# Performance work log

Hardware: AMD Instinct MI355X
Metric: run time of the kernel (lower is better)

## Reference

```python
import jax, jax.numpy as jnp
import numpy as np

B, S, D = 2, 2048, 1024
H = 16
DK = D // H
DFF = 4096
EPS = 1e-6


def rotate_half(x):
    x1, x2 = jnp.split(x, 2, axis=-1)
    return jnp.concatenate((-x2, x1), axis=-1)


def build_rope(dim, seq_len):
    inv_freq = 1.0 / (10000.0 ** (jnp.arange(0, dim, 2, dtype=jnp.float32) / dim))
    t = jnp.arange(seq_len, dtype=jnp.float32)
    freqs = jnp.einsum('i,j->ij', t, inv_freq)
    emb = jnp.concatenate((freqs, freqs), axis=-1)
    return jnp.cos(emb)[None, None], jnp.sin(emb)[None, None]  # [1,1,S,dk]


def rmsnorm(x, g):
    rms = jnp.sqrt(jnp.mean(x * x, axis=-1, keepdims=True) + EPS)
    return x / rms * g


def setup_inputs() -> dict:
    key = jax.random.key(0)
    ks = jax.random.split(key, 10)
    sc = 0.02
    x = jax.random.normal(ks[0], (B, S, D), dtype=jnp.float32)
    mask = jnp.tril(jnp.ones((S, S), dtype=jnp.int32))[None, None]  # causal [1,1,S,S]
    wq = jax.random.normal(ks[1], (D, D), dtype=jnp.float32) * sc
    wk = jax.random.normal(ks[2], (D, D), dtype=jnp.float32) * sc
    wv = jax.random.normal(ks[3], (D, D), dtype=jnp.float32) * sc
    wo = jax.random.normal(ks[4], (D, D), dtype=jnp.float32) * sc
    w1 = jax.random.normal(ks[5], (2 * DFF, D), dtype=jnp.float32) * sc
    w2 = jax.random.normal(ks[6], (D, DFF), dtype=jnp.float32) * sc
    g1 = jnp.ones((D,), dtype=jnp.float32)
    g2 = jnp.ones((D,), dtype=jnp.float32)
    return {"x": x, "mask": mask, "wq": wq, "wk": wk, "wv": wv, "wo": wo,
            "w1": w1, "w2": w2, "g1": g1, "g2": g2}


def decoder_block(x, mask, wq, wk, wv, wo, w1, w2, g1, g2):
    b, s, d = x.shape
    # --- self-attention sublayer ---
    h = rmsnorm(x, g1)
    q = (h @ wq.T).reshape(b, s, H, DK).transpose(0, 2, 1, 3)
    k = (h @ wk.T).reshape(b, s, H, DK).transpose(0, 2, 1, 3)
    v = (h @ wv.T).reshape(b, s, H, DK).transpose(0, 2, 1, 3)
    cos, sin = build_rope(DK, s)
    q = q * cos + rotate_half(q) * sin
    k = k * cos + rotate_half(k) * sin
    scores = jnp.einsum('bhqd,bhkd->bhqk', q, k) / jnp.sqrt(jnp.float32(DK))
    scores = jnp.where(mask == 0, jnp.float32(-1e9), scores)
    p = jax.nn.softmax(scores, axis=-1)
    ctx = jnp.einsum('bhqk,bhkd->bhqd', p, v)
    ctx = ctx.transpose(0, 2, 1, 3).reshape(b, s, d)
    x = x + ctx @ wo.T
    # --- SwiGLU FFN sublayer ---
    h2 = rmsnorm(x, g2)
    u = h2 @ w1.T  # [b,s,2*DFF]
    u1, u2 = jnp.split(u, 2, axis=-1)
    ffn = (u1 * jax.nn.silu(u2)) @ w2.T
    return x + ffn


def reference(x, mask, wq, wk, wv, wo, w1, w2, g1, g2):
    return decoder_block(x, mask, wq, wk, wv, wo, w1, w2, g1, g2)
```

## Files before the change

kernel.cpp:

```cpp
#include <hip/hip_runtime.h>
#include <hip/hip_bf16.h>

#define BB 2
#define SS 2048
#define DD 1024
#define NH 16
#define DKH 64
#define DFF 4096
#define MTOK (BB*SS)

typedef __hip_bfloat16 bf16;
typedef __attribute__((ext_vector_type(8))) short s16x8;
typedef __attribute__((ext_vector_type(4))) float f32x4;

__device__ __forceinline__ float bs2f(short s) {
    unsigned int u = ((unsigned int)(unsigned short)s) << 16;
    return __uint_as_float(u);
}
__device__ __forceinline__ float b2f(bf16 v) { return __bfloat162float(v); }
__device__ __forceinline__ bf16 f2b(float v) { return __float2bfloat16(v); }
__device__ __forceinline__ short f2bs(float v) {
    bf16 b = __float2bfloat16(v);
    return *(short*)&b;
}

__device__ __forceinline__ void load16(const bf16* g, bf16* l) {
    __builtin_amdgcn_global_load_lds((const __attribute__((address_space(1))) void*)g,
                                     (__attribute__((address_space(3))) void*)l,
                                     16, 0, 0);
}


__global__ void cvt_kernel(const float* __restrict__ src, bf16* __restrict__ dst) {
    const int i = blockIdx.x * blockDim.x + threadIdx.x;
    float4 v = ((const float4*)src)[i];
    short4 o;
    o.x = f2bs(v.x); o.y = f2bs(v.y); o.z = f2bs(v.z); o.w = f2bs(v.w);
    ((short4*)dst)[i] = o;
}

__global__ void cvt4_kernel(const float* __restrict__ s0, const float* __restrict__ s1,
                            const float* __restrict__ s2, const float* __restrict__ s3,
                            bf16* __restrict__ dst) {
    const int z = blockIdx.z;
    const float* src = (z == 0) ? s0 : (z == 1) ? s1 : (z == 2) ? s2 : s3;
    const int i = blockIdx.x * blockDim.x + threadIdx.x;
    float4 v = ((const float4*)src)[i];
    short4 o;
    o.x = f2bs(v.x); o.y = f2bs(v.y); o.z = f2bs(v.z); o.w = f2bs(v.w);
    ((short4*)(dst + (size_t)z * DD * DD))[i] = o;
}

__global__ void rmsnorm_kernel(const float* __restrict__ x, const float* __restrict__ g,
                               bf16* __restrict__ out) {
    const int row = blockIdx.x;
    const int tid = threadIdx.x;
    float4 xv = ((const float4*)(x + (size_t)row * DD))[tid];
    float ss = xv.x*xv.x + xv.y*xv.y + xv.z*xv.z + xv.w*xv.w;
    #pragma unroll
    for (int off = 32; off > 0; off >>= 1) ss += __shfl_down(ss, off);
    __shared__ float red[4];
    const int wv = tid >> 6, lane = tid & 63;
    if (lane == 0) red[wv] = ss;
    __syncthreads();
    const float tot = red[0] + red[1] + red[2] + red[3];
    const float inv = rsqrtf(tot * (1.0f / DD) + 1e-6f);
    float4 gv = ((const float4*)g)[tid];
    short4 o;
    o.x = f2bs(xv.x * inv * gv.x);
    o.y = f2bs(xv.y * inv * gv.y);
    o.z = f2bs(xv.z * inv * gv.z);
    o.w = f2bs(xv.w * inv * gv.w);
    ((short4*)(out + (size_t)row * DD))[tid] = o;
}

__global__ __launch_bounds__(256) void gemm_qkv(const bf16* __restrict__ A,
                                                const bf16* __restrict__ Wbase,
                                                bf16* __restrict__ Obase) {
    __shared__ bf16 As[128 * 32];
    __shared__ bf16 Bs[128 * 32];
    const int tid = threadIdx.x, lane = tid & 63, wv = tid >> 6;
    const int col = lane & 15, quad = lane >> 4;
    const int wm = wv >> 1, wn = wv & 1;
    const int m0 = blockIdx.y * 128;
    const int n0 = blockIdx.x * 128;
    const bf16* W = Wbase + (size_t)blockIdx.z * DD * DD;
    bf16* C = Obase + (size_t)blockIdx.z * MTOK * DD;

    const int srow = tid >> 2;
    const int scol = (((tid & 3) ^ (srow & 3))) * 8;
    const bf16* Ag = A + (size_t)(m0 + srow) * DD + scol;
    const bf16* Wg = W + (size_t)(n0 + srow) * DD + scol;
    bf16* Asl = As + tid * 8;
    bf16* Bsl = Bs + tid * 8;
    const size_t half = (size_t)64 * DD;
    const int rg = (quad ^ (col & 3)) * 8;

    f32x4 acc[4][4] = {};
    for (int k0 = 0; k0 < DD; k0 += 32) {
        __syncthreads();
        load16(Ag + k0,        Asl);
        load16(Ag + half + k0, Asl + 2048);
        load16(Wg + k0,        Bsl);
        load16(Wg + half + k0, Bsl + 2048);
        __syncthreads();
        s16x8 af[4], bfr[4];
        #pragma unroll
        for (int t = 0; t < 4; t++) {
            af[t]  = *(const s16x8*)(As + (wm * 64 + t * 16 + col) * 32 + rg);
            bfr[t] = *(const s16x8*)(Bs + (wn * 64 + t * 16 + col) * 32 + rg);
        }
        #pragma unroll
        for (int tm = 0; tm < 4; tm++)
            #pragma unroll
            for (int tn = 0; tn < 4; tn++)
                acc[tm][tn] = __builtin_amdgcn_mfma_f32_16x16x32_bf16(af[tm], bfr[tn], acc[tm][tn], 0, 0, 0);
    }
    #pragma unroll
    for (int tm = 0; tm < 4; tm++)
        #pragma unroll
        for (int tn = 0; tn < 4; tn++)
            #pragma unroll
            for (int r = 0; r < 4; r++) {
                const int rr = m0 + wm * 64 + tm * 16 + quad * 4 + r;
                const int cc = n0 + wn * 64 + tn * 16 + col;
                C[(size_t)rr * DD + cc] = f2b(acc[tm][tn][r]);
            }
}

__global__ __launch_bounds__(256) void gemm128_atomic(const bf16* __restrict__ A,
                                                      const bf16* __restrict__ W,
                                                      float* C, int N, int K, int KC) {
    __shared__ bf16 As[128 * 32];
    __shared__ bf16 Bs[128 * 32];
    const int tid = threadIdx.x, lane = tid & 63, wv = tid >> 6;
    const int col = lane & 15, quad = lane >> 4;
    const int wm = wv >> 1, wn = wv & 1;
    const int m0 = blockIdx.y * 128;
    const int n0 = blockIdx.x * 128;
    const int koff = blockIdx.z * KC;

    const int srow = tid >> 2;
    const int scol = (((tid & 3) ^ (srow & 3))) * 8;
    const bf16* Ag = A + (size_t)(m0 + srow) * K + scol;
    const bf16* Wg = W + (size_t)(n0 + srow) * K + scol;
    bf16* Asl = As + tid * 8;
    bf16* Bsl = Bs + tid * 8;
    const size_t half = (size_t)64 * K;
    const int rg = (quad ^ (col & 3)) * 8;

    f32x4 acc[4][4] = {};
    for (int k0 = koff; k0 < koff + KC; k0 += 32) {
        __syncthreads();
        load16(Ag + k0,        Asl);
        load16(Ag + half + k0, Asl + 2048);
        load16(Wg + k0,        Bsl);
        load16(Wg + half + k0, Bsl + 2048);
        __syncthreads();
        s16x8 af[4], bfr[4];
        #pragma unroll
        for (int t = 0; t < 4; t++) {
            af[t]  = *(const s16x8*)(As + (wm * 64 + t * 16 + col) * 32 + rg);
            bfr[t] = *(const s16x8*)(Bs + (wn * 64 + t * 16 + col) * 32 + rg);
        }
        #pragma unroll
        for (int tm = 0; tm < 4; tm++)
            #pragma unroll
            for (int tn = 0; tn < 4; tn++)
                acc[tm][tn] = __builtin_amdgcn_mfma_f32_16x16x32_bf16(af[tm], bfr[tn], acc[tm][tn], 0, 0, 0);
    }
    #pragma unroll
    for (int tm = 0; tm < 4; tm++)
        #pragma unroll
        for (int tn = 0; tn < 4; tn++)
            #pragma unroll
            for (int r = 0; r < 4; r++) {
                const int rr = m0 + wm * 64 + tm * 16 + quad * 4 + r;
                const int cc = n0 + wn * 64 + tn * 16 + col;
                atomicAdd(&C[(size_t)rr * N + cc], acc[tm][tn][r]);
            }
}

__global__ __launch_bounds__(256) void gemm64n_f32res(const bf16* __restrict__ A,
                                                      const bf16* __restrict__ W,
                                                      const float* res, float* C,
                                                      int M, int N, int K) {
    __shared__ bf16 As[128 * 32];
    __shared__ bf16 Bs[64 * 32];
    const int tid = threadIdx.x, lane = tid & 63, wv = tid >> 6;
    const int col = lane & 15, quad = lane >> 4;
    const int wm = wv >> 1, wn = wv & 1;
    const int m0 = blockIdx.y * 128;
    const int n0 = blockIdx.x * 64;

    const int srow = tid >> 2;
    const int scol = (((tid & 3) ^ (srow & 3))) * 8;
    const bf16* Ag = A + (size_t)(m0 + srow) * K + scol;
    const bf16* Wg = W + (size_t)(n0 + srow) * K + scol;
    bf16* Asl = As + tid * 8;
    bf16* Bsl = Bs + tid * 8;
    const size_t half = (size_t)64 * K;
    const int rg = (quad ^ (col & 3)) * 8;

    f32x4 acc[4][2] = {};
    for (int k0 = 0; k0 < K; k0 += 32) {
        __syncthreads();
        load16(Ag + k0,        Asl);
        load16(Ag + half + k0, Asl + 2048);
        load16(Wg + k0,        Bsl);
        __syncthreads();
        s16x8 af[4], bfr[2];
        #pragma unroll
        for (int t = 0; t < 4; t++)
            af[t] = *(const s16x8*)(As + (wm * 64 + t * 16 + col) * 32 + rg);
        #pragma unroll
        for (int t = 0; t < 2; t++)
            bfr[t] = *(const s16x8*)(Bs + (wn * 32 + t * 16 + col) * 32 + rg);
        #pragma unroll
        for (int tm = 0; tm < 4; tm++)
            #pragma unroll
            for (int tn = 0; tn < 2; tn++)
                acc[tm][tn] = __builtin_amdgcn_mfma_f32_16x16x32_bf16(af[tm], bfr[tn], acc[tm][tn], 0, 0, 0);
    }
    #pragma unroll
    for (int tm = 0; tm < 4; tm++)
        #pragma unroll
        for (int tn = 0; tn < 2; tn++)
            #pragma unroll
            for (int r = 0; r < 4; r++) {
                const int rr = m0 + wm * 64 + tm * 16 + quad * 4 + r;
                const int cc = n0 + wn * 32 + tn * 16 + col;
                C[(size_t)rr * N + cc] = acc[tm][tn][r] + res[(size_t)rr * N + cc];
            }
}

__device__ __forceinline__ void stage_sw(const bf16* Ag, const bf16* Wg0, const bf16* Wg1,
                                         bf16* Asl, bf16* Bsl, int k0) {
    load16(Ag + k0,                        Asl);
    load16(Ag + k0 + 32,                   Asl + 8192);
    load16(Ag + (size_t)128 * DD + k0,     Asl + 4096);
    load16(Ag + (size_t)128 * DD + k0 + 32, Asl + 8192 + 4096);
    load16(Wg0 + k0,                       Bsl);
    load16(Wg0 + k0 + 32,                  Bsl + 8192);
    load16(Wg1 + k0,                       Bsl + 4096);
    load16(Wg1 + k0 + 32,                  Bsl + 8192 + 4096);
}

__device__ __forceinline__ void compute_sw(const bf16* Ab, const bf16* Bb,
                                           f32x4 (*acc)[4],
                                           int wm, int wn, int col, int quad) {
    const int rg = (quad ^ (col & 3)) * 8;
    #pragma unroll
    for (int kk = 0; kk < 2; kk++) {
        const bf16* Ap = Ab + kk * 8192;
        const bf16* Bp = Bb + kk * 8192;
        s16x8 af[8], bfr[4];
        #pragma unroll
        for (int t = 0; t < 8; t++)
            af[t] = *(const s16x8*)(Ap + (wm * 128 + t * 16 + col) * 32 + rg);
        #pragma unroll
        for (int t = 0; t < 4; t++)
            bfr[t] = *(const s16x8*)(Bp + (wn * 64 + t * 16 + col) * 32 + rg);
        #pragma unroll
        for (int tm = 0; tm < 8; tm++)
            #pragma unroll
            for (int tn = 0; tn < 4; tn++)
                acc[tm][tn] = __builtin_amdgcn_mfma_f32_16x16x32_bf16(af[tm], bfr[tn], acc[tm][tn], 0, 0, 0);
    }
}

__global__ __launch_bounds__(512, 2) void gemm256_swiglu(const bf16* __restrict__ A,
                                                         const bf16* __restrict__ W,
                                                         bf16* __restrict__ G) {
    __shared__ bf16 As[2][2][256 * 32];
    __shared__ bf16 Bs[2][2][256 * 32];
    const int tid = threadIdx.x, lane = tid & 63, wv = tid >> 6;
    const int col = lane & 15, quad = lane >> 4;
    const int wm = wv >> 2, wn = wv & 3;
    const int m0 = blockIdx.y * 256;
    const int n0 = blockIdx.x * 128;

    const int srow = tid >> 2;
    const int scol = ((tid & 3) ^ (srow & 3)) * 8;
    const bf16* Ag = A + (size_t)(m0 + srow) * DD + scol;
    const int r0 = srow, r1 = srow + 128;
    const int wr0 = n0 + ((r0 >> 6) << 5) + (r0 & 31) + (((r0 >> 5) & 1) ? DFF : 0);
    const int wr1 = n0 + ((r1 >> 6) << 5) + (r1 & 31) + (((r1 >> 5) & 1) ? DFF : 0);
    const bf16* Wg0 = W + (size_t)wr0 * DD + scol;
    const bf16* Wg1 = W + (size_t)wr1 * DD + scol;
    bf16* Asl = &As[0][0][0] + tid * 8;
    bf16* Bsl = &Bs[0][0][0] + tid * 8;
    const int bufoff = 2 * 8192;

    f32x4 acc[8][4] = {};

    stage_sw(Ag, Wg0, Wg1, Asl, Bsl, 0);
    __syncthreads();
    int buf = 0;
    for (int t = 0; t < 15; t++) {
        stage_sw(Ag, Wg0, Wg1, Asl + (buf ^ 1) * bufoff, Bsl + (buf ^ 1) * bufoff,
                 (t + 1) * 64);
        compute_sw(&As[buf][0][0], &Bs[buf][0][0], acc, wm, wn, col, quad);
        __syncthreads();
        buf ^= 1;
    }
    compute_sw(&As[buf][0][0], &Bs[buf][0][0], acc, wm, wn, col, quad);

    #pragma unroll
    for (int tm = 0; tm < 8; tm++)
        #pragma unroll
        for (int tn = 0; tn < 2; tn++)
            #pragma unroll
            for (int r = 0; r < 4; r++) {
                const int rr = m0 + wm * 128 + tm * 16 + quad * 4 + r;
                const int cc = n0 + wn * 32 + tn * 16 + col;
                const float u1 = acc[tm][tn][r];
                const float u2 = acc[tm][tn + 2][r];
                const float sig = 1.0f / (1.0f + __expf(-u2));
                G[(size_t)rr * DFF + cc] = f2b(u1 * u2 * sig);
            }
}

__global__ void rope_kernel(bf16* __restrict__ q, bf16* __restrict__ k) {
    const int idx = blockIdx.x * blockDim.x + threadIdx.x;
    const int d = idx & 31;
    const int h = (idx >> 5) & (NH - 1);
    const int row = idx >> 9;
    const int s = row & (SS - 1);
    const float invf = powf(10000.0f, -(float)d * (1.0f / 32.0f));
    const float ang = (float)s * invf;
    float sn, cs;
    sincosf(ang, &sn, &cs);
    const size_t base = (size_t)row * DD + h * DKH + d;
    {
        float x1 = b2f(q[base]), x2 = b2f(q[base + 32]);
        q[base]      = f2b(x1 * cs - x2 * sn);
        q[base + 32] = f2b(x2 * cs + x1 * sn);
    }
    {
        float x1 = b2f(k[base]), x2 = b2f(k[base + 32]);
        k[base]      = f2b(x1 * cs - x2 * sn);
        k[base + 32] = f2b(x2 * cs + x1 * sn);
    }
}

__global__ __launch_bounds__(256) void vt_transpose(const bf16* __restrict__ v,
                                                    bf16* __restrict__ vt) {
    __shared__ short tile[64][72];
    const int s0 = blockIdx.x * 64;
    const int bh = blockIdx.y;
    const int b = bh >> 4, h = bh & 15;
    const bf16* src = v + (size_t)b * SS * DD + h * DKH;
    #pragma unroll
    for (int it = 0; it < 2; it++) {
        const int sl = (threadIdx.x >> 3) + it * 32;
        const int dp = (threadIdx.x & 7) * 8;
        s16x8 val = *(const s16x8*)(src + (size_t)(s0 + sl) * DD + dp);
        *(s16x8*)&tile[sl][dp] = val;
    }
    __syncthreads();
    bf16* dst = vt + (size_t)bh * DKH * SS;
    #pragma unroll
    for (int it = 0; it < 2; it++) {
        const int dk = (threadIdx.x >> 3) + it * 32;
        const int sp = (threadIdx.x & 7) * 8;
        s16x8 o;
        #pragma unroll
        for (int j = 0; j < 8; j++) o[j] = tile[sp + j][dk];
        *(s16x8*)(dst + (size_t)dk * SS + s0 + sp) = o;
    }
}

__device__ __forceinline__ void stage_kv(const bf16* kbase, const bf16* vtbase,
                                         bf16* Kd, bf16* Vd, int kt0, int tid) {
    const int row0 = tid >> 3;
    const int gl = tid & 7;
    #pragma unroll
    for (int r = 0; r < 2; r++) {
        const int row = row0 + r * 32;
        const int g = (gl ^ (row & 7)) * 8;
        load16(kbase + (size_t)(kt0 + row) * DD + g, Kd + tid * 8 + r * 2048);
        load16(vtbase + (size_t)row * SS + kt0 + g,  Vd + tid * 8 + r * 2048);
    }
}

__device__ __forceinline__ void attn_step(const bf16* Ks, const bf16* Vs,
                                          short (*pl)[72],
                                          s16x8 qf0, s16x8 qf1,
                                          f32x4* cacc, float* lacc,
                                          int col, int quad, int kt0, int q0w,
                                          bool need_mask) {
    f32x4 s4[4] = {};
    #pragma unroll
    for (int t = 0; t < 4; t++) {
        const int key = 16 * t + col;
        const int g0 = (quad ^ (key & 7)) * 8;
        s16x8 b0 = *(const s16x8*)(Ks + key * 64 + g0);
        s16x8 b1 = *(const s16x8*)(Ks + key * 64 + (g0 ^ 32));
        s4[t] = __builtin_amdgcn_mfma_f32_16x16x32_bf16(qf0, b0, s4[t], 0, 0, 0);
        s4[t] = __builtin_amdgcn_mfma_f32_16x16x32_bf16(qf1, b1, s4[t], 0, 0, 0);
    }
    #pragma unroll
    for (int t = 0; t < 4; t++)
        #pragma unroll
        for (int r = 0; r < 4; r++) {
            float sv = s4[t][r] * 0.125f;
            if (need_mask) {
                const int key = kt0 + 16 * t + col;
                const int qq  = q0w + quad * 4 + r;
                if (key > qq) sv = -1.0e30f;
            }
            const float p = __expf(sv);
            s4[t][r] = p;
            lacc[r] += p;
        }
    #pragma unroll
    for (int t = 0; t < 4; t++)
        #pragma unroll
        for (int r = 0; r < 4; r++)
            pl[quad * 4 + r][col + 16 * t] = f2bs(s4[t][r]);
    s16x8 pf0 = *(const s16x8*)&pl[col][quad * 8];
    s16x8 pf1 = *(const s16x8*)&pl[col][32 + quad * 8];
    #pragma unroll
    for (int tn = 0; tn < 4; tn++) {
        const int dk = 16 * tn + col;
        const int g0 = (quad ^ (dk & 7)) * 8;
        s16x8 b0 = *(const s16x8*)(Vs + dk * 64 + g0);
        s16x8 b1 = *(const s16x8*)(Vs + dk * 64 + (g0 ^ 32));
        cacc[tn] = __builtin_amdgcn_mfma_f32_16x16x32_bf16(pf0, b0, cacc[tn], 0, 0, 0);
        cacc[tn] = __builtin_amdgcn_mfma_f32_16x16x32_bf16(pf1, b1, cacc[tn], 0, 0, 0);
    }
}

__global__ __launch_bounds__(256) void attn_mfma2(const bf16* __restrict__ q,
                                                  const bf16* __restrict__ k,
                                                  const bf16* __restrict__ vt,
                                                  bf16* __restrict__ ctx) {
    __shared__ bf16 Ks[2][64 * 64];
    __shared__ bf16 Vs[2][64 * 64];
    __shared__ short plds[4][16][72];
    const int tid = threadIdx.x, lane = tid & 63, wv = tid >> 6;
    const int col = lane & 15, quad = lane >> 4;
    const int bh = blockIdx.y;
    const int b = bh >> 4, h = bh & 15;
    const int tA = blockIdx.x;
    const int tB = 31 - tA;
    const int q0A = tA * 64 + wv * 16;
    const int q0B = tB * 64 + wv * 16;

    const bf16* kbase  = k  + (size_t)b * SS * DD + h * DKH;
    const bf16* vtbase = vt + (size_t)bh * DKH * SS;

    const bf16* qrA = q + (size_t)(b * SS + q0A + col) * DD + h * DKH + quad * 8;
    const bf16* qrB = q + (size_t)(b * SS + q0B + col) * DD + h * DKH + quad * 8;
    s16x8 qfA0 = *(const s16x8*)(qrA);
    s16x8 qfA1 = *(const s16x8*)(qrA + 32);
    s16x8 qfB0 = *(const s16x8*)(qrB);
    s16x8 qfB1 = *(const s16x8*)(qrB + 32);

    f32x4 caccA[4] = {}, caccB[4] = {};
    float lA[4] = {}, lB[4] = {};

    const int last = tB;
    stage_kv(kbase, vtbase, Ks[0], Vs[0], 0, tid);
    int buf = 0;
    for (int kt = 0; kt <= last; kt++) {
        __syncthreads();
        if (kt < last)
            stage_kv(kbase, vtbase, Ks[buf ^ 1], Vs[buf ^ 1], (kt + 1) * 64, tid);
        const bf16* Kc = Ks[buf];
        const bf16* Vc = Vs[buf];
        if (kt <= tA)
            attn_step(Kc, Vc, plds[wv], qfA0, qfA1, caccA, lA,
                      col, quad, kt * 64, q0A, kt == tA);
        attn_step(Kc, Vc, plds[wv], qfB0, qfB1, caccB, lB,
                  col, quad, kt * 64, q0B, kt == tB);
        buf ^= 1;
    }
    #pragma unroll
    for (int r = 0; r < 4; r++) {
        #pragma unroll
        for (int off = 1; off < 16; off <<= 1) {
            lA[r] += __shfl_xor(lA[r], off);
            lB[r] += __shfl_xor(lB[r], off);
        }
    }
    #pragma unroll
    for (int tn = 0; tn < 4; tn++)
        #pragma unroll
        for (int r = 0; r < 4; r++) {
            const size_t tokA = (size_t)(b * SS + q0A + quad * 4 + r);
            ctx[tokA * DD + h * DKH + 16 * tn + col] = f2b(caccA[tn][r] / lA[r]);
            const size_t tokB = (size_t)(b * SS + q0B + quad * 4 + r);
            ctx[tokB * DD + h * DKH + 16 * tn + col] = f2b(caccB[tn][r] / lB[r]);
        }
}

extern "C" void kernel_launch(void* const* d_in, const int* in_sizes, int n_in,
                              void* d_out, int out_size, void* d_ws, size_t ws_size,
                              hipStream_t stream) {
    const float* x  = (const float*)d_in[0];
    const float* wq = (const float*)d_in[2];
    const float* wk = (const float*)d_in[3];
    const float* wv = (const float*)d_in[4];
    const float* wo = (const float*)d_in[5];
    const float* w1 = (const float*)d_in[6];
    const float* w2 = (const float*)d_in[7];
    const float* g1 = (const float*)d_in[8];
    const float* g2 = (const float*)d_in[9];
    float* out = (float*)d_out;
    char* ws = (char*)d_ws;

    const size_t MB = 1024 * 1024;
    bf16* hb   = (bf16*)(ws + 0 * MB);
    bf16* qb   = (bf16*)(ws + 8 * MB);
    bf16* kb   = (bf16*)(ws + 16 * MB);
    bf16* vb   = (bf16*)(ws + 24 * MB);
    bf16* ctxb = hb;
    bf16* h2b  = hb;
    bf16* gb   = qb;
    bf16* wqb  = (bf16*)(ws + 32 * MB);
    bf16* wob  = wqb + (size_t)3 * DD * DD;
    bf16* vtb  = (bf16*)(ws + 40 * MB);
    bf16* w1b  = (bf16*)(ws + 40 * MB);
    bf16* w2b  = (bf16*)(ws + 56 * MB);

    cvt4_kernel<<<dim3((DD * DD / 4) / 256, 1, 4), 256, 0, stream>>>(
        wq, wk, wv, wo, wqb);

    rmsnorm_kernel<<<MTOK, 256, 0, stream>>>(x, g1, hb);
    gemm_qkv<<<dim3(DD / 128, MTOK / 128, 3), 256, 0, stream>>>(hb, wqb, qb);

    vt_transpose<<<dim3(SS / 64, BB * NH), 256, 0, stream>>>(vb, vtb);
    rope_kernel<<<(BB * SS * NH * 32) / 256, 256, 0, stream>>>(qb, kb);

    attn_mfma2<<<dim3(16, BB * NH), 256, 0, stream>>>(qb, kb, vtb, ctxb);

    gemm64n_f32res<<<dim3(DD / 64, MTOK / 128), 256, 0, stream>>>(
        ctxb, wob, x, out, MTOK, DD, DD);
    rmsnorm_kernel<<<MTOK, 256, 0, stream>>>(out, g2, h2b);

    cvt_kernel<<<(2 * DFF * DD / 4) / 256, 256, 0, stream>>>(w1, w1b);
    cvt_kernel<<<(DD * DFF / 4) / 256, 256, 0, stream>>>(w2, w2b);

    gemm256_swiglu<<<dim3(DFF / 128, MTOK / 256), 512, 0, stream>>>(h2b, w1b, gb);
    gemm128_atomic<<<dim3(DD / 128, MTOK / 128, 2), 256, 0, stream>>>(
        gb, w2b, out, DD, DFF, DFF / 2);
}
```

Baseline: 440.5 us.

## Use 4-stage K32 LDS ring with vmcnt waits in SwiGLU GEMM

```diff
diff --git a/kernel.cpp b/kernel.cpp
--- a/kernel.cpp
+++ b/kernel.cpp
@@ -29,6 +29,8 @@
                                      (__attribute__((address_space(3))) void*)l,
                                      16, 0, 0);
 }
+
+#define WAITV(N) asm volatile("s_waitcnt vmcnt(" #N ")" ::: "memory")
 
 
 __global__ void cvt_kernel(const float* __restrict__ src, bf16* __restrict__ dst) {
@@ -234,46 +236,40 @@
             }
 }
 
-__device__ __forceinline__ void stage_sw(const bf16* Ag, const bf16* Wg0, const bf16* Wg1,
-                                         bf16* Asl, bf16* Bsl, int k0) {
-    load16(Ag + k0,                        Asl);
-    load16(Ag + k0 + 32,                   Asl + 8192);
-    load16(Ag + (size_t)128 * DD + k0,     Asl + 4096);
-    load16(Ag + (size_t)128 * DD + k0 + 32, Asl + 8192 + 4096);
-    load16(Wg0 + k0,                       Bsl);
-    load16(Wg0 + k0 + 32,                  Bsl + 8192);
-    load16(Wg1 + k0,                       Bsl + 4096);
-    load16(Wg1 + k0 + 32,                  Bsl + 8192 + 4096);
-}
-
-__device__ __forceinline__ void compute_sw(const bf16* Ab, const bf16* Bb,
-                                           f32x4 (*acc)[4],
-                                           int wm, int wn, int col, int quad) {
+__device__ __forceinline__ void stage_k32(const bf16* Ag, const bf16* Wg0,
+                                          const bf16* Wg1, bf16* Abuf, bf16* Bbuf,
+                                          int k0, int tid) {
+    load16(Ag + k0,                    Abuf + tid * 8);
+    load16(Ag + (size_t)128 * DD + k0, Abuf + tid * 8 + 4096);
+    load16(Wg0 + k0,                   Bbuf + tid * 8);
+    load16(Wg1 + k0,                   Bbuf + tid * 8 + 4096);
+}
+
+__device__ __forceinline__ void comp_k32(const bf16* Ap, const bf16* Bp,
+                                         f32x4 (*acc)[4],
+                                         int wm, int wn, int col, int quad) {
     const int rg = (quad ^ (col & 3)) * 8;
-    #pragma unroll
-    for (int kk = 0; kk < 2; kk++) {
-        const bf16* Ap = Ab + kk * 8192;
-        const bf16* Bp = Bb + kk * 8192;
-        s16x8 af[8], bfr[4];
-        #pragma unroll
-        for (int t = 0; t < 8; t++)
-            af[t] = *(const s16x8*)(Ap + (wm * 128 + t * 16 + col) * 32 + rg);
-        #pragma unroll
-        for (int t = 0; t < 4; t++)
-            bfr[t] = *(const s16x8*)(Bp + (wn * 64 + t * 16 + col) * 32 + rg);
-        #pragma unroll
-        for (int tm = 0; tm < 8; tm++)
-            #pragma unroll
-            for (int tn = 0; tn < 4; tn++)
-                acc[tm][tn] = __builtin_amdgcn_mfma_f32_16x16x32_bf16(af[tm], bfr[tn], acc[tm][tn], 0, 0, 0);
-    }
+    s16x8 af[8], bfr[4];
+    #pragma unroll
+    for (int t = 0; t < 8; t++)
+        af[t] = *(const s16x8*)(Ap + (wm * 128 + t * 16 + col) * 32 + rg);
+    #pragma unroll
+    for (int t = 0; t < 4; t++)
+        bfr[t] = *(const s16x8*)(Bp + (wn * 64 + t * 16 + col) * 32 + rg);
+    __builtin_amdgcn_s_setprio(1);
+    #pragma unroll
+    for (int tm = 0; tm < 8; tm++)
+        #pragma unroll
+        for (int tn = 0; tn < 4; tn++)
+            acc[tm][tn] = __builtin_amdgcn_mfma_f32_16x16x32_bf16(af[tm], bfr[tn], acc[tm][tn], 0, 0, 0);
+    __builtin_amdgcn_s_setprio(0);
 }
 
 __global__ __launch_bounds__(512, 2) void gemm256_swiglu(const bf16* __restrict__ A,
                                                          const bf16* __restrict__ W,
                                                          bf16* __restrict__ G) {
-    __shared__ bf16 As[2][2][256 * 32];
-    __shared__ bf16 Bs[2][2][256 * 32];
+    __shared__ bf16 As[4][256 * 32];
+    __shared__ bf16 Bs[4][256 * 32];
     const int tid = threadIdx.x, lane = tid & 63, wv = tid >> 6;
     const int col = lane & 15, quad = lane >> 4;
     const int wm = wv >> 2, wn = wv & 3;
@@ -288,23 +284,32 @@
     const int wr1 = n0 + ((r1 >> 6) << 5) + (r1 & 31) + (((r1 >> 5) & 1) ? DFF : 0);
     const bf16* Wg0 = W + (size_t)wr0 * DD + scol;
     const bf16* Wg1 = W + (size_t)wr1 * DD + scol;
-    bf16* Asl = &As[0][0][0] + tid * 8;
-    bf16* Bsl = &Bs[0][0][0] + tid * 8;
-    const int bufoff = 2 * 8192;
 
     f32x4 acc[8][4] = {};
 
-    stage_sw(Ag, Wg0, Wg1, Asl, Bsl, 0);
-    __syncthreads();
-    int buf = 0;
-    for (int t = 0; t < 15; t++) {
-        stage_sw(Ag, Wg0, Wg1, Asl + (buf ^ 1) * bufoff, Bsl + (buf ^ 1) * bufoff,
-                 (t + 1) * 64);
-        compute_sw(&As[buf][0][0], &Bs[buf][0][0], acc, wm, wn, col, quad);
-        __syncthreads();
-        buf ^= 1;
-    }
-    compute_sw(&As[buf][0][0], &Bs[buf][0][0], acc, wm, wn, col, quad);
+    stage_k32(Ag, Wg0, Wg1, As[0], Bs[0], 0,  tid);
+    stage_k32(Ag, Wg0, Wg1, As[1], Bs[1], 32, tid);
+    stage_k32(Ag, Wg0, Wg1, As[2], Bs[2], 64, tid);
+
+    for (int t = 0; t < 29; t++) {
+        WAITV(8);
+        __builtin_amdgcn_s_barrier();
+        asm volatile("" ::: "memory");
+        stage_k32(Ag, Wg0, Wg1, As[(t + 3) & 3], Bs[(t + 3) & 3], (t + 3) * 32, tid);
+        comp_k32(As[t & 3], Bs[t & 3], acc, wm, wn, col, quad);
+    }
+    WAITV(8);
+    __builtin_amdgcn_s_barrier();
+    asm volatile("" ::: "memory");
+    comp_k32(As[29 & 3], Bs[29 & 3], acc, wm, wn, col, quad);
+    WAITV(4);
+    __builtin_amdgcn_s_barrier();
+    asm volatile("" ::: "memory");
+    comp_k32(As[30 & 3], Bs[30 & 3], acc, wm, wn, col, quad);
+    WAITV(0);
+    __builtin_amdgcn_s_barrier();
+    asm volatile("" ::: "memory");
+    comp_k32(As[31 & 3], Bs[31 & 3], acc, wm, wn, col, quad);
 
     #pragma unroll
     for (int tm = 0; tm < 8; tm++)
```

Result: slower. 449.6 us (+2.1%).
